# Kernel tuning notes

Hardware: AMD Instinct MI355X
Metric: run time of the kernel (lower is better)

Reference implementation:

```python
import jax, jax.numpy as jnp
import numpy as np

N_NODES = 50000
N_EDGES = 1_600_000
D_NODE = 64
D_EDGE = 16
HEADS = 4
ATT_F = 16  # features[0] / heads = 64 / 4
LN_EPS = 1e-6


def setup_inputs() -> dict:
    key = jax.random.key(0)
    ks = jax.random.split(key, 9)
    nodes = jax.random.normal(ks[0], (N_NODES, D_NODE), dtype=jnp.float32)
    edges = jax.random.normal(ks[1], (N_EDGES, D_EDGE), dtype=jnp.float32)
    receivers = jax.random.randint(ks[2], (N_EDGES,), 0, N_NODES)
    senders = jax.random.randint(ks[3], (N_EDGES,), 0, N_NODES)
    # he_normal-like scale for W (fan_in = input feature dim)
    W = jax.random.normal(ks[4], (HEADS, ATT_F, D_NODE), dtype=jnp.float32) * np.sqrt(2.0 / D_NODE)
    W_edge = jax.random.normal(ks[5], (HEADS, ATT_F, D_EDGE), dtype=jnp.float32) * np.sqrt(2.0 / D_EDGE)
    # xavier_normal-like scale for a
    a = jax.random.normal(ks[6], (HEADS, 3 * ATT_F), dtype=jnp.float32) * np.sqrt(2.0 / (HEADS + 3 * ATT_F))
    ln_scale = jnp.ones((HEADS * ATT_F,), dtype=jnp.float32)
    ln_bias = jnp.zeros((HEADS * ATT_F,), dtype=jnp.float32)
    return {"nodes": nodes, "edges": edges, "receivers": receivers, "senders": senders,
            "W": W, "W_edge": W_edge, "a": a, "ln_scale": ln_scale, "ln_bias": ln_bias}


def reference(nodes, edges, receivers, senders, W, W_edge, a, ln_scale, ln_bias):
    n = nodes.shape[0]
    # add self edges (zero edge features)
    self_idx = jnp.arange(n)
    r = jnp.concatenate([receivers, self_idx], axis=0)          # [Etot]
    s = jnp.concatenate([senders, self_idx], axis=0)            # [Etot]
    e = jnp.concatenate([edges, jnp.zeros((n, edges.shape[1]), edges.dtype)], axis=0)  # [Etot, De]

    # project node features once, then gather per edge
    Wn = jnp.einsum('hfi,ni->nhf', W, nodes)                    # [N, H, F]
    Ws = Wn[s]                                                   # [Etot, H, F]
    Wr = Wn[r]                                                   # [Etot, H, F]
    We = jnp.einsum('hfi,ei->ehf', W_edge, e)                   # [Etot, H, F]

    # attention logits: a . [Ws || Wr || We], computed without materializing the concat
    a_s, a_r, a_e = jnp.split(a, 3, axis=-1)                    # each [H, F]
    msg = (jnp.einsum('ehf,hf->eh', Ws, a_s)
           + jnp.einsum('ehf,hf->eh', Wr, a_r)
           + jnp.einsum('ehf,hf->eh', We, a_e))                 # [Etot, H]
    lm = jax.nn.leaky_relu(msg)

    # segment softmax over edges grouped by receiver
    seg_max = jax.ops.segment_max(lm, r, num_segments=n)        # [N, H]
    z = lm - seg_max[r]
    exp_z = jnp.exp(z)
    norm = jax.ops.segment_sum(exp_z, r, num_segments=n)        # [N, H]
    alpha = exp_z / norm[r]                                     # [Etot, H]

    # attention-weighted scatter-sum aggregation
    att_msg = alpha[:, :, None] * Ws                            # [Etot, H, F]
    aggr = jax.ops.segment_sum(att_msg, r, num_segments=n)      # [N, H, F]
    out = aggr.reshape(n, -1)                                   # [N, H*F]

    out = jax.nn.elu(out)
    # LayerNorm (flax default: eps=1e-6, scale & bias over last axis)
    mean = jnp.mean(out, axis=-1, keepdims=True)
    var = jnp.mean(jnp.square(out - mean), axis=-1, keepdims=True)
    out = (out - mean) * jax.lax.rsqrt(var + LN_EPS)
    out = out * ln_scale + ln_bias
    return out
```

## Files before the change

kernel.cpp:

```cpp
#include <hip/hip_runtime.h>
#include <hip/hip_fp16.h>

#define LEAKY_SLOPE 0.01f
#define LN_EPS 1e-6f
#define SUBS 8
#define CAP 352
#define MAXE (SUBS*CAP)
#define CSTRIDE 16

__device__ __forceinline__ float head_sel(int h, float a, float b, float c, float d) {
    float lo = (h & 1) ? b : a;
    float hi = (h & 1) ? d : c;
    return (h & 2) ? hi : lo;
}

__device__ __forceinline__ int xcc_id() {
    return (int)(__builtin_amdgcn_s_getreg(20 | (3 << 11)) & 7);
}

__global__ __launch_bounds__(256) void node_proj_kernel(
    const float* __restrict__ nodes, const float* __restrict__ W,
    const float* __restrict__ a, __half* __restrict__ Wn16,
    float* __restrict__ s_s, float* __restrict__ s_r,
    float* __restrict__ lm_self, int* __restrict__ cursor,
    int ncursor, int N)
{
    int t = threadIdx.x;
    int ci = blockIdx.x * 256 + t;
    if (ci < ncursor) cursor[ci] = 0;

    int lane = t & 63;
    int wv = t >> 6;
    float w[64];
    const float4* W4 = (const float4*)W;
    #pragma unroll
    for (int i = 0; i < 16; i++) {
        float4 v = W4[lane * 16 + i];
        w[4*i] = v.x; w[4*i+1] = v.y; w[4*i+2] = v.z; w[4*i+3] = v.w;
    }
    int h = lane >> 4, f = lane & 15;
    float as_ = a[h * 48 + f];
    float ar_ = a[h * 48 + 16 + f];
    int n0 = blockIdx.x * 16 + wv * 4;
    #pragma unroll
    for (int k = 0; k < 4; k++) {
        int n = n0 + k;
        if (n >= N) break;
        const float4* row4 = (const float4*)(nodes + (size_t)n * 64);
        float acc = 0.f;
        #pragma unroll
        for (int c = 0; c < 16; c++) {
            float4 v = row4[c];
            acc += v.x * w[4*c] + v.y * w[4*c+1] + v.z * w[4*c+2] + v.w * w[4*c+3];
        }
        Wn16[(size_t)n * 64 + lane] = __float2half(acc);
        float ps = acc * as_;
        float pr = acc * ar_;
        #pragma unroll
        for (int off = 1; off < 16; off <<= 1) {
            ps += __shfl_xor(ps, off);
            pr += __shfl_xor(pr, off);
        }
        if (f == 0) {
            s_s[n * 4 + h] = ps;
            s_r[n * 4 + h] = pr;
            float v = ps + pr;
            lm_self[n * 4 + h] = v > 0.f ? v : LEAKY_SLOPE * v;
        }
    }
}

__global__ __launch_bounds__(256) void edge_bin_kernel(
    const float* __restrict__ edges, const int* __restrict__ receivers,
    const int* __restrict__ senders, const float* __restrict__ W_edge,
    const float* __restrict__ a, const float* __restrict__ s_s,
    const float* __restrict__ s_r, int* __restrict__ cursor,
    int4* __restrict__ slab, int E)
{
    __shared__ float be[4][16];
    int t = threadIdx.x;
    int e = blockIdx.x * 256 + t;
    bool act = e < E;
    int r = 0, s = 0;
    if (act) { r = receivers[e]; s = senders[e]; }
    if (t < 64) {
        int h = t >> 4, i = t & 15;
        float sm = 0.f;
        #pragma unroll
        for (int f = 0; f < 16; f++)
            sm += W_edge[(h * 16 + f) * 16 + i] * a[h * 48 + 32 + f];
        be[h][i] = sm;
    }
    __syncthreads();
    if (!act) return;

    int b = r >> 6;
    int cidx = b * SUBS + xcc_id();
    int slot = __hip_atomic_fetch_add(&cursor[cidx * CSTRIDE], 1,
                                      __ATOMIC_RELAXED,
                                      __HIP_MEMORY_SCOPE_WORKGROUP);

    const float4* ef = (const float4*)(edges + (size_t)e * 16);
    float4 e0 = ef[0], e1 = ef[1], e2 = ef[2], e3 = ef[3];
    float4 ssv = ((const float4*)s_s)[s];
    float4 srv = ((const float4*)s_r)[r];
    float ev[16] = {e0.x, e0.y, e0.z, e0.w, e1.x, e1.y, e1.z, e1.w,
                    e2.x, e2.y, e2.z, e2.w, e3.x, e3.y, e3.z, e3.w};
    float ssa[4] = {ssv.x, ssv.y, ssv.z, ssv.w};
    float sra[4] = {srv.x, srv.y, srv.z, srv.w};
    float lm[4];
    #pragma unroll
    for (int hh = 0; hh < 4; hh++) {
        float se = 0.f;
        #pragma unroll
        for (int i = 0; i < 16; i++) se += be[hh][i] * ev[i];
        float v = ssa[hh] + sra[hh] + se;
        lm[hh] = v > 0.f ? v : LEAKY_SLOPE * v;
    }
    if (slot < CAP) {
        unsigned packA = (unsigned)__half_as_ushort(__float2half(lm[2])) |
                         ((unsigned)__half_as_ushort(__float2half(lm[3])) << 16);
        unsigned packB = (unsigned)s | ((unsigned)(r & 63) << 16);
        slab[(size_t)cidx * CAP + slot] =
            make_int4(__float_as_int(lm[0]), __float_as_int(lm[1]),
                      (int)packA, (int)packB);
    }
}

__global__ __launch_bounds__(256) void bucket_sort_kernel(
    const int* __restrict__ cursor, int4* __restrict__ slab,
    int2* __restrict__ meta, int N)
{
    __shared__ int4 raw[MAXE];
    __shared__ unsigned short perm[MAXE];
    __shared__ int cnt64[64];
    __shared__ int off64[64];
    __shared__ int cur64[64];

    int b = blockIdx.x;
    int t = threadIdx.x;
    int nn = min(64, N - b * 64);

    if (t < 64) cnt64[t] = 0;
    __syncthreads();

    int c[SUBS], basearr[SUBS];
    int tot = 0;
    #pragma unroll
    for (int sub = 0; sub < SUBS; sub++) {
        int cc = min(cursor[(b * SUBS + sub) * CSTRIDE], CAP);
        c[sub] = cc; basearr[sub] = tot; tot += cc;
    }

    #pragma unroll
    for (int sub = 0; sub < SUBS; sub++) {
        int cc = c[sub], bs = basearr[sub];
        const int4* src = slab + (size_t)(b * SUBS + sub) * CAP;
        for (int i = t; i < cc; i += 256) {
            int4 p = src[i];
            raw[bs + i] = p;
            atomicAdd(&cnt64[((unsigned)p.w >> 16) & 63], 1);
        }
    }
    __syncthreads();

    if (t < 64) {
        int v = cnt64[t];
        int incl = v;
        #pragma unroll
        for (int off = 1; off < 64; off <<= 1) {
            int u = __shfl_up(incl, off);
            if (t >= off) incl += u;
        }
        off64[t] = incl - v;
        cur64[t] = incl - v;
    }
    __syncthreads();

    for (int i = t; i < tot; i += 256) {
        int rl = ((unsigned)raw[i].w >> 16) & 63;
        int pos = atomicAdd(&cur64[rl], 1);
        perm[pos] = (unsigned short)i;
    }
    __syncthreads();

    int4* dst = slab + (size_t)b * MAXE;
    for (int pos = t; pos < tot; pos += 256)
        dst[pos] = raw[perm[pos]];

    if (t < nn)
        meta[b * 64 + t] = make_int2(b * MAXE + off64[t], cnt64[t]);
}

__global__ __launch_bounds__(256) void node_aggr_kernel(
    const __half* __restrict__ Wn16, const float* __restrict__ lm_self,
    const int2* __restrict__ meta, const int4* __restrict__ sorted,
    const float* __restrict__ ln_scale, const float* __restrict__ ln_bias,
    float* __restrict__ out, int N)
{
    __shared__ float lds_w[4][64][4];
    __shared__ int   lds_s[4][64];
    int t = threadIdx.x;
    int lane = t & 63;
    int wv = t >> 6;
    int n = blockIdx.x * 4 + wv;
    if (n >= N) return;
    int2 mt = meta[n];
    int beg = mt.x, cntn = mt.y;
    int h = lane >> 4;

    float acc = 0.f, acc2 = 0.f;
    float p0 = 0.f, p1 = 0.f, p2 = 0.f, p3 = 0.f;

    for (int base = 0; base < cntn; base += 64) {
        int j = base + lane;
        float w0 = 0.f, w1 = 0.f, w2 = 0.f, w3 = 0.f;
        int sv = 0;
        if (j < cntn) {
            int4 pl = sorted[beg + j];
            w0 = __expf(__int_as_float(pl.x));
            w1 = __expf(__int_as_float(pl.y));
            unsigned pa = (unsigned)pl.z;
            w2 = __expf(__half2float(__ushort_as_half((unsigned short)(pa & 0xFFFFu))));
            w3 = __expf(__half2float(__ushort_as_half((unsigned short)(pa >> 16))));
            sv = (int)((unsigned)pl.w & 0xFFFFu);
        }
        p0 += w0; p1 += w1; p2 += w2; p3 += w3;
        lds_s[wv][lane] = sv;
        *(float4*)&lds_w[wv][lane][0] = make_float4(w0, w1, w2, w3);
        int cnt = min(64, cntn - base);
        int k = 0;
        for (; k + 1 < cnt; k += 2) {
            int   sk0 = lds_s[wv][k];
            int   sk1 = lds_s[wv][k + 1];
            float a0  = lds_w[wv][k][h];
            float a1  = lds_w[wv][k + 1][h];
            acc  += a0 * __half2float(Wn16[(size_t)sk0 * 64 + lane]);
            acc2 += a1 * __half2float(Wn16[(size_t)sk1 * 64 + lane]);
        }
        if (k < cnt)
            acc += lds_w[wv][k][h] * __half2float(Wn16[(size_t)lds_s[wv][k] * 64 + lane]);
    }
    acc += acc2;

    #pragma unroll
    for (int off = 1; off < 64; off <<= 1) {
        p0 += __shfl_xor(p0, off);
        p1 += __shfl_xor(p1, off);
        p2 += __shfl_xor(p2, off);
        p3 += __shfl_xor(p3, off);
    }
    float4 ls = ((const float4*)lm_self)[n];
    float ws0 = __expf(ls.x), ws1 = __expf(ls.y);
    float ws2 = __expf(ls.z), ws3 = __expf(ls.w);
    float totd  = head_sel(h, p0 + ws0, p1 + ws1, p2 + ws2, p3 + ws3);
    float wself = head_sel(h, ws0, ws1, ws2, ws3);
    acc = (acc + wself * __half2float(Wn16[(size_t)n * 64 + lane])) / totd;

    float y = acc > 0.f ? acc : expm1f(acc);
    float sum = y;
    #pragma unroll
    for (int off = 1; off < 64; off <<= 1) sum += __shfl_xor(sum, off);
    float mean = sum * 0.015625f;
    float d = y - mean;
    float vs = d * d;
    #pragma unroll
    for (int off = 1; off < 64; off <<= 1) vs += __shfl_xor(vs, off);
    float var = vs * 0.015625f;
    float o = d * rsqrtf(var + LN_EPS) * ln_scale[lane] + ln_bias[lane];
    out[(size_t)n * 64 + lane] = o;
}

extern "C" void kernel_launch(void* const* d_in, const int* in_sizes, int n_in,
                              void* d_out, int out_size, void* d_ws, size_t ws_size,
                              hipStream_t stream) {
    const float* nodes     = (const float*)d_in[0];
    const float* edges     = (const float*)d_in[1];
    const int*   receivers = (const int*)d_in[2];
    const int*   senders   = (const int*)d_in[3];
    const float* W         = (const float*)d_in[4];
    const float* W_edge    = (const float*)d_in[5];
    const float* a         = (const float*)d_in[6];
    const float* ln_scale  = (const float*)d_in[7];
    const float* ln_bias   = (const float*)d_in[8];
    float* out = (float*)d_out;

    int N = in_sizes[0] / 64;
    int E = in_sizes[2];
    int NB = (N + 63) / 64;
    int ncursor = NB * SUBS * CSTRIDE;

    char* ws = (char*)d_ws;
    size_t off = 0;
    auto alloc = [&](size_t bytes) -> void* {
        void* p = ws + off;
        off += (bytes + 15) & ~(size_t)15;
        return p;
    };
    __half* Wn16   = (__half*)alloc((size_t)N * 64 * 2);
    float* s_s     = (float*)alloc((size_t)N * 4 * 4);
    float* s_r     = (float*)alloc((size_t)N * 4 * 4);
    float* lm_self = (float*)alloc((size_t)N * 4 * 4);
    int*   cursor  = (int*)alloc((size_t)ncursor * 4);
    int2*  meta    = (int2*)alloc((size_t)N * 8);
    int4*  slab    = (int4*)alloc((size_t)NB * MAXE * 16);
    (void)ws_size; (void)n_in; (void)out_size;

    node_proj_kernel<<<(N + 15) / 16, 256, 0, stream>>>(
        nodes, W, a, Wn16, s_s, s_r, lm_self, cursor, ncursor, N);
    edge_bin_kernel<<<(E + 255) / 256, 256, 0, stream>>>(
        edges, receivers, senders, W_edge, a, s_s, s_r, cursor, slab, E);
    bucket_sort_kernel<<<NB, 256, 0, stream>>>(cursor, slab, meta, N);
    node_aggr_kernel<<<(N + 3) / 4, 256, 0, stream>>>(
        Wn16, lm_self, meta, slab, ln_scale, ln_bias, out, N);
}
```

Measured before the change: 368.0 us.

## Sort edge records via a permutation index instead of moving slab records

The bucket sort no longer copies each 16-byte edge record through LDS and writes it back sorted. It reads only the receiver word, builds a 16-bit permutation per bucket and writes that to a new global buffer. The aggregation kernel then reads each record through the permutation, which turns a sequential read into an indirect one. The sort block size also grows to 512 threads, and the edge and index streams in the binning kernel use nontemporal loads.

```diff
diff --git a/kernel.cpp b/kernel.cpp
--- a/kernel.cpp
+++ b/kernel.cpp
@@ -7,6 +7,9 @@
 #define CAP 352
 #define MAXE (SUBS*CAP)
 #define CSTRIDE 16
+#define K3T 512
+
+typedef float  f4v __attribute__((ext_vector_type(4)));
 
 __device__ __forceinline__ float head_sel(int h, float a, float b, float c, float d) {
     float lo = (h & 1) ? b : a;
@@ -82,7 +85,10 @@
     int e = blockIdx.x * 256 + t;
     bool act = e < E;
     int r = 0, s = 0;
-    if (act) { r = receivers[e]; s = senders[e]; }
+    if (act) {
+        r = __builtin_nontemporal_load(receivers + e);
+        s = __builtin_nontemporal_load(senders + e);
+    }
     if (t < 64) {
         int h = t >> 4, i = t & 15;
         float sm = 0.f;
@@ -100,12 +106,15 @@
                                       __ATOMIC_RELAXED,
                                       __HIP_MEMORY_SCOPE_WORKGROUP);
 
-    const float4* ef = (const float4*)(edges + (size_t)e * 16);
-    float4 e0 = ef[0], e1 = ef[1], e2 = ef[2], e3 = ef[3];
+    const f4v* ef = (const f4v*)(edges + (size_t)e * 16);
+    f4v e0 = __builtin_nontemporal_load(ef);
+    f4v e1 = __builtin_nontemporal_load(ef + 1);
+    f4v e2 = __builtin_nontemporal_load(ef + 2);
+    f4v e3 = __builtin_nontemporal_load(ef + 3);
     float4 ssv = ((const float4*)s_s)[s];
     float4 srv = ((const float4*)s_r)[r];
-    float ev[16] = {e0.x, e0.y, e0.z, e0.w, e1.x, e1.y, e1.z, e1.w,
-                    e2.x, e2.y, e2.z, e2.w, e3.x, e3.y, e3.z, e3.w};
+    float ev[16] = {e0[0], e0[1], e0[2], e0[3], e1[0], e1[1], e1[2], e1[3],
+                    e2[0], e2[1], e2[2], e2[3], e3[0], e3[1], e3[2], e3[3]};
     float ssa[4] = {ssv.x, ssv.y, ssv.z, ssv.w};
     float sra[4] = {srv.x, srv.y, srv.z, srv.w};
     float lm[4];
@@ -127,11 +136,12 @@
     }
 }
 
-__global__ __launch_bounds__(256) void bucket_sort_kernel(
-    const int* __restrict__ cursor, int4* __restrict__ slab,
-    int2* __restrict__ meta, int N)
+__global__ __launch_bounds__(K3T) void bucket_sort_kernel(
+    const int* __restrict__ cursor, const int4* __restrict__ slab,
+    unsigned short* __restrict__ permG, int2* __restrict__ meta, int N)
 {
-    __shared__ int4 raw[MAXE];
+    __shared__ unsigned char  rl8[MAXE];
+    __shared__ unsigned short sl16[MAXE];
     __shared__ unsigned short perm[MAXE];
     __shared__ int cnt64[64];
     __shared__ int off64[64];
@@ -155,11 +165,13 @@
     #pragma unroll
     for (int sub = 0; sub < SUBS; sub++) {
         int cc = c[sub], bs = basearr[sub];
-        const int4* src = slab + (size_t)(b * SUBS + sub) * CAP;
-        for (int i = t; i < cc; i += 256) {
-            int4 p = src[i];
-            raw[bs + i] = p;
-            atomicAdd(&cnt64[((unsigned)p.w >> 16) & 63], 1);
+        const int* srcW = (const int*)(slab + (size_t)(b * SUBS + sub) * CAP);
+        for (int i = t; i < cc; i += K3T) {
+            unsigned w = (unsigned)srcW[i * 4 + 3];
+            int rl = (int)((w >> 16) & 63u);
+            rl8[bs + i]  = (unsigned char)rl;
+            sl16[bs + i] = (unsigned short)(sub * CAP + i);
+            atomicAdd(&cnt64[rl], 1);
         }
     }
     __syncthreads();
@@ -177,16 +189,16 @@
     }
     __syncthreads();
 
-    for (int i = t; i < tot; i += 256) {
-        int rl = ((unsigned)raw[i].w >> 16) & 63;
+    for (int i = t; i < tot; i += K3T) {
+        int rl = (int)rl8[i];
         int pos = atomicAdd(&cur64[rl], 1);
-        perm[pos] = (unsigned short)i;
-    }
-    __syncthreads();
-
-    int4* dst = slab + (size_t)b * MAXE;
-    for (int pos = t; pos < tot; pos += 256)
-        dst[pos] = raw[perm[pos]];
+        perm[pos] = sl16[i];
+    }
+    __syncthreads();
+
+    unsigned short* pg = permG + (size_t)b * MAXE;
+    for (int pos = t; pos < tot; pos += K3T)
+        pg[pos] = perm[pos];
 
     if (t < nn)
         meta[b * 64 + t] = make_int2(b * MAXE + off64[t], cnt64[t]);
@@ -194,7 +206,8 @@
 
 __global__ __launch_bounds__(256) void node_aggr_kernel(
     const __half* __restrict__ Wn16, const float* __restrict__ lm_self,
-    const int2* __restrict__ meta, const int4* __restrict__ sorted,
+    const int2* __restrict__ meta, const int4* __restrict__ slab,
+    const unsigned short* __restrict__ permG,
     const float* __restrict__ ln_scale, const float* __restrict__ ln_bias,
     float* __restrict__ out, int N)
 {
@@ -208,6 +221,7 @@
     int2 mt = meta[n];
     int beg = mt.x, cntn = mt.y;
     int h = lane >> 4;
+    const int4* slabB = slab + (size_t)(n >> 6) * MAXE;
 
     float acc = 0.f, acc2 = 0.f;
     float p0 = 0.f, p1 = 0.f, p2 = 0.f, p3 = 0.f;
@@ -217,7 +231,8 @@
         float w0 = 0.f, w1 = 0.f, w2 = 0.f, w3 = 0.f;
         int sv = 0;
         if (j < cntn) {
-            int4 pl = sorted[beg + j];
+            int slot = (int)permG[beg + j];
+            int4 pl = slabB[slot];
             w0 = __expf(__int_as_float(pl.x));
             w1 = __expf(__int_as_float(pl.y));
             unsigned pa = (unsigned)pl.z;
@@ -303,6 +318,7 @@
     float* lm_self = (float*)alloc((size_t)N * 4 * 4);
     int*   cursor  = (int*)alloc((size_t)ncursor * 4);
     int2*  meta    = (int2*)alloc((size_t)N * 8);
+    unsigned short* permG = (unsigned short*)alloc((size_t)NB * MAXE * 2);
     int4*  slab    = (int4*)alloc((size_t)NB * MAXE * 16);
     (void)ws_size; (void)n_in; (void)out_size;
 
@@ -310,7 +326,7 @@
         nodes, W, a, Wn16, s_s, s_r, lm_self, cursor, ncursor, N);
     edge_bin_kernel<<<(E + 255) / 256, 256, 0, stream>>>(
         edges, receivers, senders, W_edge, a, s_s, s_r, cursor, slab, E);
-    bucket_sort_kernel<<<NB, 256, 0, stream>>>(cursor, slab, meta, N);
+    bucket_sort_kernel<<<NB, K3T, 0, stream>>>(cursor, slab, permG, meta, N);
     node_aggr_kernel<<<(N + 3) / 4, 256, 0, stream>>>(
-        Wn16, lm_self, meta, slab, ln_scale, ln_bias, out, N);
-}
+        Wn16, lm_self, meta, slab, permG, ln_scale, ln_bias, out, N);
+}
```

After: 384.4 us. +4.4%, slower.
